# Performance work log

Hardware: AMD Instinct MI355X
Metric: run time of the kernel (lower is better)

## Reference

```python
import jax, jax.numpy as jnp
import numpy as np

B, F, N = 16, 64, 32768
C0, C1, C2 = 64, 16, 1
TOP_K = 64
EPS = 1e-5


def setup_inputs() -> dict:
    key = jax.random.key(0)
    ks = jax.random.split(key, 6)
    def rn(k, shape, scale=1.0):
        return jax.random.normal(k, shape, dtype=jnp.float32) * scale
    return {
        "sortvec": rn(ks[0], (B, 1, F, N)),
        "input": rn(ks[1], (B, F, N)),
        # conv0: kernel (F,1), in=1, out=64 -> weight reduces to [C0, F]
        "w0": rn(ks[2], (C0, F), np.sqrt(2.0 / F)), "b0": jnp.zeros((C0,), jnp.float32),
        "w1": rn(ks[3], (C1, C0), np.sqrt(2.0 / C0)), "b1": jnp.zeros((C1,), jnp.float32),
        "w2": rn(ks[4], (C2, C1), np.sqrt(2.0 / C1)), "b2": jnp.zeros((C2,), jnp.float32),
        "g0": jnp.ones((C0,), jnp.float32), "bt0": jnp.zeros((C0,), jnp.float32),
        "g1": jnp.ones((C1,), jnp.float32), "bt1": jnp.zeros((C1,), jnp.float32),
        "g2": jnp.ones((C2,), jnp.float32), "bt2": jnp.zeros((C2,), jnp.float32),
    }


def _bn_relu(x, g, b):
    # training-mode BatchNorm2d over (B, N) per channel; x: [B, C, N]
    mu = jnp.mean(x, axis=(0, 2), keepdims=True)
    var = jnp.var(x, axis=(0, 2), keepdims=True)
    return jax.nn.relu((x - mu) * jax.lax.rsqrt(var + EPS) * g[None, :, None] + b[None, :, None])


def reference(sortvec, input, w0, b0, w1, b1, w2, b2, g0, bt0, g1, bt1, g2, bt2):
    # conv0 with kernel (F,1) collapses the feature axis: [B,1,F,N] -> [B,C0,N]
    x = jnp.einsum('bfn,of->bon', sortvec[:, 0], w0) + b0[None, :, None]
    x = _bn_relu(x, g0, bt0)
    x = _bn_relu(jnp.einsum('bcn,oc->bon', x, w1) + b1[None, :, None], g1, bt1)
    score = _bn_relu(jnp.einsum('bcn,oc->bon', x, w2) + b2[None, :, None], g2, bt2)  # [B,1,N]
    _, idx = jax.lax.top_k(score[:, 0], TOP_K)                                        # [B,K]
    sorted_input = jnp.take_along_axis(input, idx[:, None, :], axis=2)                # [B,F,K]
    sorted_score = jnp.take_along_axis(score, idx[:, None, :], axis=2)                # [B,1,K]
    feat = jnp.concatenate([sorted_input, sorted_score], axis=1)                      # [B,F+1,K]
    return feat, idx
```

## Files before the change

### kernel.cpp

```cpp
#include <hip/hip_runtime.h>


constexpr int   B_   = 16;
constexpr int   N_   = 32768;
constexpr int   K_   = 64;
constexpr long long S_ = (long long)B_ * N_;
constexpr float EPS_ = 1e-5f;

constexpr int T128  = 4096;
constexpr int NB0   = 2048;
constexpr int NB1   = 2048;
constexpr int NB2   = 256;
constexpr int NBC   = 128;
constexpr int NBINS = 4096;
constexpr int CAP   = 1024;

__device__ __forceinline__ unsigned key_map(float f) {
  unsigned u = __float_as_uint(f);
  return (u & 0x80000000u) ? ~u : (u | 0x80000000u);
}

__global__ __launch_bounds__(256) void k_prep(const float* __restrict__ w0,
                                              const float* __restrict__ w1,
                                              float* __restrict__ w0T,
                                              float* __restrict__ w1T) {
  int t = threadIdx.x;
  for (int e = t; e < 64 * 64; e += 256) {
    int o = e >> 6, f = e & 63;
    w0T[f * 64 + o] = w0[e];
  }
  for (int e = t; e < 16 * 64; e += 256) {
    int o = e >> 6, c = e & 63;
    w1T[c * 16 + o] = w1[e];
  }
}

__global__ __launch_bounds__(256) void k_stat0(const float* __restrict__ sv,
                                               const float* __restrict__ w0T,
                                               const float* __restrict__ b0,
                                               float* __restrict__ p0) {
  __shared__ float svt[64][128];
  const int t  = threadIdx.x;
  const int p  = t & 63;
  const int cg = __builtin_amdgcn_readfirstlane(t >> 6);

  float bb[16];
#pragma unroll
  for (int j = 0; j < 16; ++j) bb[j] = b0[cg * 16 + j];

  float s1[16], s2[16];
#pragma unroll
  for (int j = 0; j < 16; ++j) { s1[j] = 0.f; s2[j] = 0.f; }

  for (int tile = blockIdx.x; tile < T128; tile += NB0) {
    const int b  = tile >> 8;
    const int n0 = (tile & 255) << 7;
    const float* src = sv + ((long long)b * 64) * N_ + n0;
    __syncthreads();
#pragma unroll
    for (int q = 0; q < 8; ++q) {
      int e = t + q * 256;
      int f = e >> 5, c4 = (e & 31) << 2;
      *(float4*)&svt[f][c4] = *(const float4*)(src + (long long)f * N_ + c4);
    }
    __syncthreads();

    float2 y[16];
#pragma unroll
    for (int j = 0; j < 16; ++j) { y[j].x = bb[j]; y[j].y = bb[j]; }
    for (int f = 0; f < 64; ++f) {
      const float2 x = *(const float2*)&svt[f][p << 1];
      const float* wr = w0T + f * 64 + cg * 16;
#pragma unroll
      for (int j = 0; j < 16; ++j) {
        y[j].x = fmaf(wr[j], x.x, y[j].x);
        y[j].y = fmaf(wr[j], x.y, y[j].y);
      }
    }
#pragma unroll
    for (int j = 0; j < 16; ++j) {
      s1[j] += y[j].x + y[j].y;
      s2[j] = fmaf(y[j].x, y[j].x, fmaf(y[j].y, y[j].y, s2[j]));
    }
  }

#pragma unroll
  for (int j = 0; j < 16; ++j) {
#pragma unroll
    for (int off = 32; off; off >>= 1) {
      s1[j] += __shfl_down(s1[j], off, 64);
      s2[j] += __shfl_down(s2[j], off, 64);
    }
  }
  if (p == 0) {
    float* dst = p0 + (long long)blockIdx.x * 128;
#pragma unroll
    for (int j = 0; j < 16; ++j) {
      dst[cg * 16 + j]      = s1[j];
      dst[64 + cg * 16 + j] = s2[j];
    }
  }
}

__global__ __launch_bounds__(1024) void k_reduce0(const float* __restrict__ p0,
                                                  const float* __restrict__ g,
                                                  const float* __restrict__ bt,
                                                  float* __restrict__ st) {
  __shared__ float l[8][128];
  const int t = threadIdx.x;
  const int j = t & 127, grp = t >> 7;
  float a0 = 0.f, a1 = 0.f, a2 = 0.f, a3 = 0.f;
  for (int i = grp; i < 512; i += 8) {
    a0 += p0[(long long)i * 128 + j];
    a1 += p0[(long long)(i + 512) * 128 + j];
    a2 += p0[(long long)(i + 1024) * 128 + j];
    a3 += p0[(long long)(i + 1536) * 128 + j];
  }
  l[grp][j] = (a0 + a1) + (a2 + a3);
  __syncthreads();
  if (t < 128) {
    float v = ((l[0][t] + l[1][t]) + (l[2][t] + l[3][t])) +
              ((l[4][t] + l[5][t]) + (l[6][t] + l[7][t]));
    l[0][t] = v;
  }
  __syncthreads();
  if (t < 64) {
    const float inv = 1.f / (float)S_;
    float mean = l[0][t] * inv;
    float ex2  = l[0][64 + t] * inv;
    float var  = ex2 - mean * mean;
    float sc   = g[t] * rsqrtf(var + EPS_);
    st[t]      = sc;
    st[64 + t] = bt[t] - mean * sc;
  }
}

__global__ __launch_bounds__(256) void k_layer01(const float* __restrict__ sv,
                                                 const float* __restrict__ w0T,
                                                 const float* __restrict__ b0,
                                                 const float* __restrict__ st0,
                                                 const float* __restrict__ w1T,
                                                 const float* __restrict__ b1,
                                                 float* __restrict__ y1,
                                                 float* __restrict__ p1) {
  __shared__ float buf[64][128];
  const int t  = threadIdx.x;
  const int p  = t & 63;
  const int cg = __builtin_amdgcn_readfirstlane(t >> 6);

  float bb[16], sc[16], sh[16];
#pragma unroll
  for (int j = 0; j < 16; ++j) {
    bb[j] = b0[cg * 16 + j];
    sc[j] = st0[cg * 16 + j];
    sh[j] = st0[64 + cg * 16 + j];
  }
  float bb1[4];
#pragma unroll
  for (int j = 0; j < 4; ++j) bb1[j] = b1[cg * 4 + j];

  float sA[4], qA[4];
#pragma unroll
  for (int j = 0; j < 4; ++j) { sA[j] = 0.f; qA[j] = 0.f; }

  for (int tile = blockIdx.x; tile < T128; tile += NB1) {
    const int b  = tile >> 8;
    const int n0 = (tile & 255) << 7;
    const float* src = sv + ((long long)b * 64) * N_ + n0;
    __syncthreads();
#pragma unroll
    for (int q = 0; q < 8; ++q) {
      int e = t + q * 256;
      int f = e >> 5, c4 = (e & 31) << 2;
      *(float4*)&buf[f][c4] = *(const float4*)(src + (long long)f * N_ + c4);
    }
    __syncthreads();

    float2 y[16];
#pragma unroll
    for (int j = 0; j < 16; ++j) { y[j].x = bb[j]; y[j].y = bb[j]; }
    for (int f = 0; f < 64; ++f) {
      const float2 x = *(const float2*)&buf[f][p << 1];
      const float* wr = w0T + f * 64 + cg * 16;
#pragma unroll
      for (int j = 0; j < 16; ++j) {
        y[j].x = fmaf(wr[j], x.x, y[j].x);
        y[j].y = fmaf(wr[j], x.y, y[j].y);
      }
    }
    __syncthreads();

#pragma unroll
    for (int j = 0; j < 16; ++j) {
      float2 h;
      h.x = fmaf(y[j].x, sc[j], sh[j]); h.x = h.x > 0.f ? h.x : 0.f;
      h.y = fmaf(y[j].y, sc[j], sh[j]); h.y = h.y > 0.f ? h.y : 0.f;
      *(float2*)&buf[cg * 16 + j][p << 1] = h;
    }
    __syncthreads();

    float2 z[4];
#pragma unroll
    for (int j = 0; j < 4; ++j) { z[j].x = bb1[j]; z[j].y = bb1[j]; }
    for (int c = 0; c < 64; ++c) {
      const float2 h = *(const float2*)&buf[c][p << 1];
      const float* wr = w1T + c * 16 + cg * 4;
#pragma unroll
      for (int j = 0; j < 4; ++j) {
        z[j].x = fmaf(wr[j], h.x, z[j].x);
        z[j].y = fmaf(wr[j], h.y, z[j].y);
      }
    }

    float* yo = y1 + ((long long)(b * 16 + cg * 4)) * N_ + n0 + (p << 1);
#pragma unroll
    for (int j = 0; j < 4; ++j) {
      *(float2*)(yo + (long long)j * N_) = z[j];
      sA[j] += z[j].x + z[j].y;
      qA[j] = fmaf(z[j].x, z[j].x, fmaf(z[j].y, z[j].y, qA[j]));
    }
  }

#pragma unroll
  for (int j = 0; j < 4; ++j) {
#pragma unroll
    for (int off = 32; off; off >>= 1) {
      sA[j] += __shfl_down(sA[j], off, 64);
      qA[j] += __shfl_down(qA[j], off, 64);
    }
  }
  if (p == 0) {
    float* dst = p1 + (long long)blockIdx.x * 32;
#pragma unroll
    for (int j = 0; j < 4; ++j) {
      dst[cg * 4 + j]      = sA[j];
      dst[16 + cg * 4 + j] = qA[j];
    }
  }
}

__global__ __launch_bounds__(1024) void k_reduce1(const float* __restrict__ p1,
                                                  const float* __restrict__ g,
                                                  const float* __restrict__ bt,
                                                  float* __restrict__ st) {
  __shared__ float l[32][32];
  const int t = threadIdx.x;
  const int j = t & 31, grp = t >> 5;
  float a0 = 0.f, a1 = 0.f;
  for (int i = grp; i < 1024; i += 32) {
    a0 += p1[(long long)i * 32 + j];
    a1 += p1[(long long)(i + 1024) * 32 + j];
  }
  l[grp][j] = a0 + a1;
  __syncthreads();
  if (t < 32) {
    float v = 0.f;
#pragma unroll
    for (int g2 = 0; g2 < 32; ++g2) v += l[g2][t];
    l[0][t] = v;
  }
  __syncthreads();
  if (t < 16) {
    const float inv = 1.f / (float)S_;
    float mean = l[0][t] * inv;
    float ex2  = l[0][16 + t] * inv;
    float var  = ex2 - mean * mean;
    float sc   = g[t] * rsqrtf(var + EPS_);
    st[t]      = sc;
    st[16 + t] = bt[t] - mean * sc;
  }
}

__global__ __launch_bounds__(1024) void k_layer2(const float* __restrict__ y1,
                                                 const float* __restrict__ st1,
                                                 const float* __restrict__ w2,
                                                 const float* __restrict__ b2,
                                                 float* __restrict__ y2,
                                                 float* __restrict__ p2,
                                                 int* __restrict__ ghist) {
  __shared__ int hist[NBINS];
  __shared__ float ls[16], lq[16];
  const int t   = threadIdx.x;
  const int blk = blockIdx.x;
  const int b   = blk >> 4;
  const int n0  = ((blk & 15) << 11) | (t << 1);

#pragma unroll
  for (int i = 0; i < NBINS / 1024; ++i) hist[t + i * 1024] = 0;

  float sc[16], sh[16], w[16];
#pragma unroll
  for (int c = 0; c < 16; ++c) { sc[c] = st1[c]; sh[c] = st1[16 + c]; w[c] = w2[c]; }
  const float bias = b2[0];

  float a0 = bias, a1 = bias;
  const float* base = y1 + ((long long)b * 16) * N_ + n0;
#pragma unroll
  for (int c = 0; c < 16; ++c) {
    float2 v = *(const float2*)(base + (long long)c * N_);
    float h;
    h = fmaf(v.x, sc[c], sh[c]); h = h > 0.f ? h : 0.f; a0 = fmaf(w[c], h, a0);
    h = fmaf(v.y, sc[c], sh[c]); h = h > 0.f ? h : 0.f; a1 = fmaf(w[c], h, a1);
  }
  float2 o; o.x = a0; o.y = a1;
  *(float2*)(y2 + (long long)b * N_ + n0) = o;

  __syncthreads();

  atomicAdd(&hist[key_map(a0) >> 20], 1);
  atomicAdd(&hist[key_map(a1) >> 20], 1);

  float ss = a0 + a1;
  float sq = fmaf(a0, a0, a1 * a1);
#pragma unroll
  for (int off = 32; off; off >>= 1) {
    ss += __shfl_down(ss, off, 64);
    sq += __shfl_down(sq, off, 64);
  }
  const int wid = t >> 6, lid = t & 63;
  if (lid == 0) { ls[wid] = ss; lq[wid] = sq; }
  __syncthreads();
  if (t == 0) {
    float Sv = 0.f, Qv = 0.f;
#pragma unroll
    for (int i = 0; i < 16; ++i) { Sv += ls[i]; Qv += lq[i]; }
    p2[blk * 2 + 0] = Sv;
    p2[blk * 2 + 1] = Qv;
  }
#pragma unroll
  for (int i = 0; i < NBINS / 1024; ++i) {
    int v = hist[t + i * 1024];
    if (v) atomicAdd(&ghist[b * NBINS + t + i * 1024], v);
  }
}

__global__ __launch_bounds__(256) void k_thresh(const int* __restrict__ ghist,
                                                int* __restrict__ Tb) {
  __shared__ int hl[NBINS + NBINS / 64];
  const int t = threadIdx.x, b = blockIdx.x;
  const int* h = ghist + b * NBINS;
  for (int i = t; i < NBINS; i += 256) hl[i + (i >> 6)] = h[i];
  __syncthreads();
  if (t < 64) {
    const int l = t;
    int s = 0;
    for (int j = 0; j < 64; ++j) s += hl[(l * 64 + j) + l];
    int Sv = s;
#pragma unroll
    for (int off = 1; off < 64; off <<= 1) {
      int v = __shfl_down(Sv, off, 64);
      if (l + off < 64) Sv += v;
    }
    unsigned long long m = __ballot(Sv >= K_);
    const int lstar = 63 - __builtin_clzll(m);
    const int tailS = (lstar < 63) ? __shfl(Sv, lstar + 1, 64) : 0;
    int Tj = hl[(lstar * 64 + l) + lstar];
#pragma unroll
    for (int off = 1; off < 64; off <<= 1) {
      int v = __shfl_down(Tj, off, 64);
      if (l + off < 64) Tj += v;
    }
    const int cge = Tj + tailS;
    unsigned long long m2 = __ballot(cge >= K_);
    const int jstar = 63 - __builtin_clzll(m2);
    if (l == 0) Tb[b] = lstar * 64 + jstar;
  }
}

__global__ __launch_bounds__(1024) void k_compact(const float* __restrict__ y2,
                                                  const int* __restrict__ Tb,
                                                  int* __restrict__ cnt,
                                                  unsigned long long* __restrict__ cand) {
  const int t = threadIdx.x, blk = blockIdx.x;
  const int b  = blk >> 3;
  const int n0 = ((blk & 7) << 12) | (t << 2);
  const int T  = Tb[b];
  float4 v = *(const float4*)(y2 + (long long)b * N_ + n0);
  unsigned long long* cb = cand + (long long)b * CAP;
#define DO_CAND(comp, off)                                                    \
  {                                                                           \
    unsigned u = key_map(comp);                                               \
    if ((int)(u >> 20) >= T) {                                                \
      int slot = atomicAdd(&cnt[b], 1);                                       \
      if (slot < CAP)                                                         \
        cb[slot] = ((unsigned long long)u << 32) |                            \
                   (unsigned)(N_ - 1 - (n0 + off));                           \
    }                                                                         \
  }
  DO_CAND(v.x, 0) DO_CAND(v.y, 1) DO_CAND(v.z, 2) DO_CAND(v.w, 3)
#undef DO_CAND
}

__global__ __launch_bounds__(64) void k_final(const unsigned long long* __restrict__ cand,
                                              const int* __restrict__ cnt,
                                              const float* __restrict__ p2,
                                              const float* __restrict__ g2,
                                              const float* __restrict__ bt2,
                                              const float* __restrict__ inp,
                                              float* __restrict__ out) {
  const int b = blockIdx.x, l = threadIdx.x;

  float s1 = (p2[2 * l] + p2[2 * (l + 64)]) +
             (p2[2 * (l + 128)] + p2[2 * (l + 192)]);
  float q1 = (p2[2 * l + 1] + p2[2 * (l + 64) + 1]) +
             (p2[2 * (l + 128) + 1] + p2[2 * (l + 192) + 1]);
#pragma unroll
  for (int off = 32; off; off >>= 1) {
    s1 += __shfl_down(s1, off, 64);
    q1 += __shfl_down(q1, off, 64);
  }
  s1 = __shfl(s1, 0, 64);
  q1 = __shfl(q1, 0, 64);
  const float inv = 1.f / (float)S_;
  const float mean = s1 * inv;
  const float var  = q1 * inv - mean * mean;
  const float scale2 = g2[0] * rsqrtf(var + EPS_);
  const float shift2 = bt2[0] - mean * scale2;

  int cn = cnt[b];
  if (cn > CAP) cn = CAP;
  const unsigned long long* cb = cand + (long long)b * CAP;
  unsigned long long k[16];
#pragma unroll
  for (int r = 0; r < 16; ++r) {
    int i = l + r * 64;
    k[r] = (i < cn) ? cb[i] : 0ull;
  }
  unsigned long long cur = 0ull;
#pragma unroll
  for (int r = 0; r < 16; ++r) cur = k[r] > cur ? k[r] : cur;

  int myidx = 0;
  unsigned mymap = 0;
  for (int r = 0; r < K_; ++r) {
    unsigned long long m = cur;
#pragma unroll
    for (int off = 32; off; off >>= 1) {
      unsigned long long o = __shfl_xor(m, off, 64);
      m = o > m ? o : m;
    }
    if (r == l) {
      myidx = N_ - 1 - (int)(m & 0xffffffffu);
      mymap = (unsigned)(m >> 32);
    }
    if (cur == m) {
#pragma unroll
      for (int r2 = 0; r2 < 16; ++r2)
        if (k[r2] == m) k[r2] = 0ull;
      unsigned long long c2 = 0ull;
#pragma unroll
      for (int r2 = 0; r2 < 16; ++r2) c2 = k[r2] > c2 ? k[r2] : c2;
      cur = c2;
    }
  }

  unsigned u = mymap;
  u = (u & 0x80000000u) ? (u & 0x7fffffffu) : ~u;
  float v = __uint_as_float(u);
  float scv = fmaf(v, scale2, shift2);
  scv = scv > 0.f ? scv : 0.f;

  const float* ib = inp + ((long long)b * 64) * N_;
#pragma unroll 4
  for (int f = 0; f < 64; ++f)
    out[((long long)b * 65 + f) * 64 + l] = ib[(long long)f * N_ + myidx];
  out[((long long)b * 65 + 64) * 64 + l] = scv;
  out[(long long)B_ * 65 * 64 + b * 64 + l] = (float)myidx;
}

extern "C" void kernel_launch(void* const* d_in, const int* in_sizes, int n_in,
                              void* d_out, int out_size, void* d_ws, size_t ws_size,
                              hipStream_t stream) {
  const float* sv  = (const float*)d_in[0];
  const float* inp = (const float*)d_in[1];
  const float* w0  = (const float*)d_in[2];
  const float* b0  = (const float*)d_in[3];
  const float* w1  = (const float*)d_in[4];
  const float* b1  = (const float*)d_in[5];
  const float* w2  = (const float*)d_in[6];
  const float* b2  = (const float*)d_in[7];
  const float* g0  = (const float*)d_in[8];
  const float* bt0 = (const float*)d_in[9];
  const float* g1  = (const float*)d_in[10];
  const float* bt1 = (const float*)d_in[11];
  const float* g2  = (const float*)d_in[12];
  const float* bt2 = (const float*)d_in[13];
  float* out = (float*)d_out;

  float* ws  = (float*)d_ws;
  float* y1  = ws;
  float* y2  = y1 + (size_t)S_ * 16;
  float* p0  = y2 + (size_t)S_;
  float* p1  = p0 + (size_t)NB0 * 128;
  float* p2  = p1 + (size_t)NB1 * 32;
  float* st0 = p2 + (size_t)NB2 * 2;
  float* st1 = st0 + 128;
  float* w0T = st1 + 32;
  float* w1T = w0T + 4096;
  int*   ghist = (int*)(w1T + 1024);
  int*   cnt   = ghist + (size_t)B_ * NBINS;
  int*   Tb    = cnt + 16;
  unsigned long long* cand =
      (unsigned long long*)(Tb + 16);

  hipMemsetAsync(ghist, 0, ((size_t)B_ * NBINS + 16) * sizeof(int), stream);

  k_prep   <<<1,    256, 0, stream>>>(w0, w1, w0T, w1T);
  k_stat0  <<<NB0,  256, 0, stream>>>(sv, w0T, b0, p0);
  k_reduce0<<<1,   1024, 0, stream>>>(p0, g0, bt0, st0);
  k_layer01<<<NB1,  256, 0, stream>>>(sv, w0T, b0, st0, w1T, b1, y1, p1);
  k_reduce1<<<1,   1024, 0, stream>>>(p1, g1, bt1, st1);
  k_layer2 <<<NB2, 1024, 0, stream>>>(y1, st1, w2, b2, y2, p2, ghist);
  k_thresh <<<B_,   256, 0, stream>>>(ghist, Tb);
  k_compact<<<NBC, 1024, 0, stream>>>(y2, Tb, cnt, cand);
  k_final  <<<B_,    64, 0, stream>>>(cand, cnt, p2, g2, bt2, inp, out);
}
```

Baseline: 292.8 us.

## Drop LDS staging of sortvec; read directly per wave with 8 channels each

The conv0 stages in k_stat0 and k_layer01 stop staging the sortvec tile through shared memory. Each of eight waves now loads its float2 column slice straight from global memory and computes 8 output channels instead of 16. Blocks grow to 512 threads and the grid halves to 1024, and the partial-sum reductions are resized to match. This removes the LDS round-trip and a barrier per tile, but every wave in a block now re-reads the same 64x128 input tile from global/L2, which multiplies global load traffic by the number of waves.

```diff
diff --git a/kernel.cpp b/kernel.cpp
--- a/kernel.cpp
+++ b/kernel.cpp
@@ -8,8 +8,8 @@
 constexpr float EPS_ = 1e-5f;
 
 constexpr int T128  = 4096;
-constexpr int NB0   = 2048;
-constexpr int NB1   = 2048;
+constexpr int NS0B  = 1024;
+constexpr int NL1B  = 1024;
 constexpr int NB2   = 256;
 constexpr int NBC   = 128;
 constexpr int NBINS = 4096;
@@ -35,69 +35,61 @@
   }
 }
 
-__global__ __launch_bounds__(256) void k_stat0(const float* __restrict__ sv,
+__global__ __launch_bounds__(512) void k_stat0(const float* __restrict__ sv,
                                                const float* __restrict__ w0T,
                                                const float* __restrict__ b0,
                                                float* __restrict__ p0) {
-  __shared__ float svt[64][128];
-  const int t  = threadIdx.x;
-  const int p  = t & 63;
-  const int cg = __builtin_amdgcn_readfirstlane(t >> 6);
-
-  float bb[16];
-#pragma unroll
-  for (int j = 0; j < 16; ++j) bb[j] = b0[cg * 16 + j];
-
-  float s1[16], s2[16];
-#pragma unroll
-  for (int j = 0; j < 16; ++j) { s1[j] = 0.f; s2[j] = 0.f; }
-
-  for (int tile = blockIdx.x; tile < T128; tile += NB0) {
+  const int t    = threadIdx.x;
+  const int lane = t & 63;
+  const int g    = __builtin_amdgcn_readfirstlane(t >> 6);
+
+  float bb[8];
+#pragma unroll
+  for (int j = 0; j < 8; ++j) bb[j] = b0[g * 8 + j];
+
+  float s1[8], s2[8];
+#pragma unroll
+  for (int j = 0; j < 8; ++j) { s1[j] = 0.f; s2[j] = 0.f; }
+
+  for (int tile = blockIdx.x; tile < T128; tile += NS0B) {
     const int b  = tile >> 8;
     const int n0 = (tile & 255) << 7;
-    const float* src = sv + ((long long)b * 64) * N_ + n0;
-    __syncthreads();
-#pragma unroll
-    for (int q = 0; q < 8; ++q) {
-      int e = t + q * 256;
-      int f = e >> 5, c4 = (e & 31) << 2;
-      *(float4*)&svt[f][c4] = *(const float4*)(src + (long long)f * N_ + c4);
-    }
-    __syncthreads();
-
-    float2 y[16];
-#pragma unroll
-    for (int j = 0; j < 16; ++j) { y[j].x = bb[j]; y[j].y = bb[j]; }
+    const float* xp = sv + ((long long)b * 64) * N_ + n0 + (lane << 1);
+
+    float2 y[8];
+#pragma unroll
+    for (int j = 0; j < 8; ++j) { y[j].x = bb[j]; y[j].y = bb[j]; }
+#pragma unroll
     for (int f = 0; f < 64; ++f) {
-      const float2 x = *(const float2*)&svt[f][p << 1];
-      const float* wr = w0T + f * 64 + cg * 16;
-#pragma unroll
-      for (int j = 0; j < 16; ++j) {
+      const float2 x = *(const float2*)(xp + (long long)f * N_);
+      const float* wr = w0T + f * 64 + g * 8;
+#pragma unroll
+      for (int j = 0; j < 8; ++j) {
         y[j].x = fmaf(wr[j], x.x, y[j].x);
         y[j].y = fmaf(wr[j], x.y, y[j].y);
       }
     }
 #pragma unroll
-    for (int j = 0; j < 16; ++j) {
+    for (int j = 0; j < 8; ++j) {
       s1[j] += y[j].x + y[j].y;
       s2[j] = fmaf(y[j].x, y[j].x, fmaf(y[j].y, y[j].y, s2[j]));
     }
   }
 
 #pragma unroll
-  for (int j = 0; j < 16; ++j) {
+  for (int j = 0; j < 8; ++j) {
 #pragma unroll
     for (int off = 32; off; off >>= 1) {
       s1[j] += __shfl_down(s1[j], off, 64);
       s2[j] += __shfl_down(s2[j], off, 64);
     }
   }
-  if (p == 0) {
+  if (lane == 0) {
     float* dst = p0 + (long long)blockIdx.x * 128;
 #pragma unroll
-    for (int j = 0; j < 16; ++j) {
-      dst[cg * 16 + j]      = s1[j];
-      dst[64 + cg * 16 + j] = s2[j];
+    for (int j = 0; j < 8; ++j) {
+      dst[g * 8 + j]      = s1[j];
+      dst[64 + g * 8 + j] = s2[j];
     }
   }
 }
@@ -110,11 +102,11 @@
   const int t = threadIdx.x;
   const int j = t & 127, grp = t >> 7;
   float a0 = 0.f, a1 = 0.f, a2 = 0.f, a3 = 0.f;
-  for (int i = grp; i < 512; i += 8) {
+  for (int i = grp; i < 256; i += 8) {
     a0 += p0[(long long)i * 128 + j];
-    a1 += p0[(long long)(i + 512) * 128 + j];
-    a2 += p0[(long long)(i + 1024) * 128 + j];
-    a3 += p0[(long long)(i + 1536) * 128 + j];
+    a1 += p0[(long long)(i + 256) * 128 + j];
+    a2 += p0[(long long)(i + 512) * 128 + j];
+    a3 += p0[(long long)(i + 768) * 128 + j];
   }
   l[grp][j] = (a0 + a1) + (a2 + a3);
   __syncthreads();
@@ -135,7 +127,7 @@
   }
 }
 
-__global__ __launch_bounds__(256) void k_layer01(const float* __restrict__ sv,
+__global__ __launch_bounds__(512) void k_layer01(const float* __restrict__ sv,
                                                  const float* __restrict__ w0T,
                                                  const float* __restrict__ b0,
                                                  const float* __restrict__ st0,
@@ -143,99 +135,84 @@
                                                  const float* __restrict__ b1,
                                                  float* __restrict__ y1,
                                                  float* __restrict__ p1) {
-  __shared__ float buf[64][128];
-  const int t  = threadIdx.x;
-  const int p  = t & 63;
-  const int cg = __builtin_amdgcn_readfirstlane(t >> 6);
-
-  float bb[16], sc[16], sh[16];
-#pragma unroll
-  for (int j = 0; j < 16; ++j) {
-    bb[j] = b0[cg * 16 + j];
-    sc[j] = st0[cg * 16 + j];
-    sh[j] = st0[64 + cg * 16 + j];
-  }
-  float bb1[4];
-#pragma unroll
-  for (int j = 0; j < 4; ++j) bb1[j] = b1[cg * 4 + j];
-
-  float sA[4], qA[4];
-#pragma unroll
-  for (int j = 0; j < 4; ++j) { sA[j] = 0.f; qA[j] = 0.f; }
-
-  for (int tile = blockIdx.x; tile < T128; tile += NB1) {
+  __shared__ float h0[64][128];
+  const int t    = threadIdx.x;
+  const int lane = t & 63;
+  const int g    = __builtin_amdgcn_readfirstlane(t >> 6);
+
+  float bb[8], sc[8], sh[8];
+#pragma unroll
+  for (int j = 0; j < 8; ++j) {
+    bb[j] = b0[g * 8 + j];
+    sc[j] = st0[g * 8 + j];
+    sh[j] = st0[64 + g * 8 + j];
+  }
+  const float b10 = b1[2 * g], b11 = b1[2 * g + 1];
+
+  float sA0 = 0.f, qA0 = 0.f, sA1 = 0.f, qA1 = 0.f;
+
+  for (int tile = blockIdx.x; tile < T128; tile += NL1B) {
     const int b  = tile >> 8;
     const int n0 = (tile & 255) << 7;
-    const float* src = sv + ((long long)b * 64) * N_ + n0;
-    __syncthreads();
-#pragma unroll
-    for (int q = 0; q < 8; ++q) {
-      int e = t + q * 256;
-      int f = e >> 5, c4 = (e & 31) << 2;
-      *(float4*)&buf[f][c4] = *(const float4*)(src + (long long)f * N_ + c4);
-    }
-    __syncthreads();
-
-    float2 y[16];
-#pragma unroll
-    for (int j = 0; j < 16; ++j) { y[j].x = bb[j]; y[j].y = bb[j]; }
+    const float* xp = sv + ((long long)b * 64) * N_ + n0 + (lane << 1);
+
+    float2 y[8];
+#pragma unroll
+    for (int j = 0; j < 8; ++j) { y[j].x = bb[j]; y[j].y = bb[j]; }
+#pragma unroll
     for (int f = 0; f < 64; ++f) {
-      const float2 x = *(const float2*)&buf[f][p << 1];
-      const float* wr = w0T + f * 64 + cg * 16;
-#pragma unroll
-      for (int j = 0; j < 16; ++j) {
+      const float2 x = *(const float2*)(xp + (long long)f * N_);
+      const float* wr = w0T + f * 64 + g * 8;
+#pragma unroll
+      for (int j = 0; j < 8; ++j) {
         y[j].x = fmaf(wr[j], x.x, y[j].x);
         y[j].y = fmaf(wr[j], x.y, y[j].y);
       }
     }
+
     __syncthreads();
-
-#pragma unroll
-    for (int j = 0; j < 16; ++j) {
+#pragma unroll
+    for (int j = 0; j < 8; ++j) {
       float2 h;
       h.x = fmaf(y[j].x, sc[j], sh[j]); h.x = h.x > 0.f ? h.x : 0.f;
       h.y = fmaf(y[j].y, sc[j], sh[j]); h.y = h.y > 0.f ? h.y : 0.f;
-      *(float2*)&buf[cg * 16 + j][p << 1] = h;
+      *(float2*)&h0[g * 8 + j][lane << 1] = h;
     }
     __syncthreads();
 
-    float2 z[4];
-#pragma unroll
-    for (int j = 0; j < 4; ++j) { z[j].x = bb1[j]; z[j].y = bb1[j]; }
+    float2 z0, z1;
+    z0.x = b10; z0.y = b10; z1.x = b11; z1.y = b11;
+#pragma unroll
     for (int c = 0; c < 64; ++c) {
-      const float2 h = *(const float2*)&buf[c][p << 1];
-      const float* wr = w1T + c * 16 + cg * 4;
-#pragma unroll
-      for (int j = 0; j < 4; ++j) {
-        z[j].x = fmaf(wr[j], h.x, z[j].x);
-        z[j].y = fmaf(wr[j], h.y, z[j].y);
-      }
-    }
-
-    float* yo = y1 + ((long long)(b * 16 + cg * 4)) * N_ + n0 + (p << 1);
-#pragma unroll
-    for (int j = 0; j < 4; ++j) {
-      *(float2*)(yo + (long long)j * N_) = z[j];
-      sA[j] += z[j].x + z[j].y;
-      qA[j] = fmaf(z[j].x, z[j].x, fmaf(z[j].y, z[j].y, qA[j]));
-    }
-  }
-
-#pragma unroll
-  for (int j = 0; j < 4; ++j) {
-#pragma unroll
-    for (int off = 32; off; off >>= 1) {
-      sA[j] += __shfl_down(sA[j], off, 64);
-      qA[j] += __shfl_down(qA[j], off, 64);
-    }
-  }
-  if (p == 0) {
+      const float2 h = *(const float2*)&h0[c][lane << 1];
+      const float* wr = w1T + c * 16 + 2 * g;
+      z0.x = fmaf(wr[0], h.x, z0.x); z0.y = fmaf(wr[0], h.y, z0.y);
+      z1.x = fmaf(wr[1], h.x, z1.x); z1.y = fmaf(wr[1], h.y, z1.y);
+    }
+
+    float* yo = y1 + ((long long)(b * 16 + 2 * g)) * N_ + n0 + (lane << 1);
+    *(float2*)yo        = z0;
+    *(float2*)(yo + N_) = z1;
+
+    sA0 += z0.x + z0.y;
+    qA0 = fmaf(z0.x, z0.x, fmaf(z0.y, z0.y, qA0));
+    sA1 += z1.x + z1.y;
+    qA1 = fmaf(z1.x, z1.x, fmaf(z1.y, z1.y, qA1));
+  }
+
+#pragma unroll
+  for (int off = 32; off; off >>= 1) {
+    sA0 += __shfl_down(sA0, off, 64);
+    qA0 += __shfl_down(qA0, off, 64);
+    sA1 += __shfl_down(sA1, off, 64);
+    qA1 += __shfl_down(qA1, off, 64);
+  }
+  if (lane == 0) {
     float* dst = p1 + (long long)blockIdx.x * 32;
-#pragma unroll
-    for (int j = 0; j < 4; ++j) {
-      dst[cg * 4 + j]      = sA[j];
-      dst[16 + cg * 4 + j] = qA[j];
-    }
+    dst[2 * g]          = sA0;
+    dst[2 * g + 1]      = sA1;
+    dst[16 + 2 * g]     = qA0;
+    dst[16 + 2 * g + 1] = qA1;
   }
 }
 
@@ -247,9 +224,9 @@
   const int t = threadIdx.x;
   const int j = t & 31, grp = t >> 5;
   float a0 = 0.f, a1 = 0.f;
-  for (int i = grp; i < 1024; i += 32) {
+  for (int i = grp; i < 512; i += 32) {
     a0 += p1[(long long)i * 32 + j];
-    a1 += p1[(long long)(i + 1024) * 32 + j];
+    a1 += p1[(long long)(i + 512) * 32 + j];
   }
   l[grp][j] = a0 + a1;
   __syncthreads();
@@ -491,8 +468,8 @@
   float* y1  = ws;
   float* y2  = y1 + (size_t)S_ * 16;
   float* p0  = y2 + (size_t)S_;
-  float* p1  = p0 + (size_t)NB0 * 128;
-  float* p2  = p1 + (size_t)NB1 * 32;
+  float* p1  = p0 + (size_t)NS0B * 128;
+  float* p2  = p1 + (size_t)NL1B * 32;
   float* st0 = p2 + (size_t)NB2 * 2;
   float* st1 = st0 + 128;
   float* w0T = st1 + 32;
@@ -505,13 +482,13 @@
 
   hipMemsetAsync(ghist, 0, ((size_t)B_ * NBINS + 16) * sizeof(int), stream);
 
-  k_prep   <<<1,    256, 0, stream>>>(w0, w1, w0T, w1T);
-  k_stat0  <<<NB0,  256, 0, stream>>>(sv, w0T, b0, p0);
-  k_reduce0<<<1,   1024, 0, stream>>>(p0, g0, bt0, st0);
-  k_layer01<<<NB1,  256, 0, stream>>>(sv, w0T, b0, st0, w1T, b1, y1, p1);
-  k_reduce1<<<1,   1024, 0, stream>>>(p1, g1, bt1, st1);
-  k_layer2 <<<NB2, 1024, 0, stream>>>(y1, st1, w2, b2, y2, p2, ghist);
-  k_thresh <<<B_,   256, 0, stream>>>(ghist, Tb);
-  k_compact<<<NBC, 1024, 0, stream>>>(y2, Tb, cnt, cand);
-  k_final  <<<B_,    64, 0, stream>>>(cand, cnt, p2, g2, bt2, inp, out);
-}
+  k_prep   <<<1,     256, 0, stream>>>(w0, w1, w0T, w1T);
+  k_stat0  <<<NS0B,  512, 0, stream>>>(sv, w0T, b0, p0);
+  k_reduce0<<<1,    1024, 0, stream>>>(p0, g0, bt0, st0);
+  k_layer01<<<NL1B,  512, 0, stream>>>(sv, w0T, b0, st0, w1T, b1, y1, p1);
+  k_reduce1<<<1,    1024, 0, stream>>>(p1, g1, bt1, st1);
+  k_layer2 <<<NB2,  1024, 0, stream>>>(y1, st1, w2, b2, y2, p2, ghist);
+  k_thresh <<<B_,    256, 0, stream>>>(ghist, Tb);
+  k_compact<<<NBC,  1024, 0, stream>>>(y2, Tb, cnt, cand);
+  k_final  <<<B_,     64, 0, stream>>>(cand, cnt, p2, g2, bt2, inp, out);
+}
```

Result: slower. 411.8 us (+40.6%).
